# Optimization experiments

Measured on AMD Instinct MI355X. Metric: run time of the kernel, lower is better.

The kernel has to match this reference:

```python
import jax, jax.numpy as jnp
import numpy as np

N_NODES = 40000
N_EDGES = 640000
IN_CH = 128
HID_CH = 128
BN_EPS = 1e-5


def setup_inputs() -> dict:
    key = jax.random.key(0)
    k_x, k_ei, k_w, k_g = jax.random.split(key, 4)
    x = jax.random.normal(k_x, (N_NODES, IN_CH), dtype=jnp.float32)
    edge_index = jax.random.randint(k_ei, (2, N_EDGES), 0, N_NODES, dtype=jnp.int32)
    # Glorot init for GCNConv weight, zero bias (PyG defaults)
    limit = float(np.sqrt(6.0 / (IN_CH + HID_CH)))
    W = jax.random.uniform(k_w, (IN_CH, HID_CH), dtype=jnp.float32, minval=-limit, maxval=limit)
    b = jnp.zeros((HID_CH,), dtype=jnp.float32)
    gamma = jnp.ones((HID_CH,), dtype=jnp.float32)
    beta = jnp.zeros((HID_CH,), dtype=jnp.float32)
    return {"x": x, "edge_index": edge_index, "W": W, "b": b, "gamma": gamma, "beta": beta}


def reference(x, edge_index, W, b, gamma, beta):
    N = x.shape[0]
    src, dst = edge_index[0], edge_index[1]

    # --- GCNConv: h = x @ W, symmetric-normalized aggregation with self-loops ---
    h = x @ W  # [N, H]
    ones = jnp.ones((src.shape[0],), dtype=x.dtype)
    deg = jax.ops.segment_sum(ones, dst, num_segments=N) + 1.0  # +1 for self-loop
    dinv = jax.lax.rsqrt(deg)  # deg >= 1 always
    norm = dinv[src] * dinv[dst]  # [E]
    msg = h[src] * norm[:, None]  # [E, H] gather
    agg = jax.ops.segment_sum(msg, dst, num_segments=N)  # scatter-add
    agg = agg + h * (dinv * dinv)[:, None]  # self-loop contribution
    out = agg + b  # bias added after aggregation (PyG GCNConv)

    # --- BatchNorm1d (training mode: batch stats, biased variance) ---
    mean = jnp.mean(out, axis=0)
    var = jnp.mean((out - mean) ** 2, axis=0)
    out = gamma * (out - mean) * jax.lax.rsqrt(var + BN_EPS) + beta

    # --- ReLU (dropout is a no-op in eval) ---
    return jax.nn.relu(out)
```

## Files before the change

kernel.cpp:

```cpp
#include <hip/hip_runtime.h>

#define N_NODES 40000
#define N_EDGES 640000
#define CH 128
#define BN_EPS 1e-5f
#define CAP 48
#define CNT_S 8
#define MM_ROWS 80
#define MM_BLOCKS (N_NODES / MM_ROWS)
#define FILL_BLOCKS (N_EDGES / 1024)


typedef __bf16 bf16x8 __attribute__((ext_vector_type(8)));
typedef float f32x4 __attribute__((ext_vector_type(4)));

__device__ __forceinline__ float bf_lo(unsigned u) { return __uint_as_float(u << 16); }
__device__ __forceinline__ float bf_hi(unsigned u) { return __uint_as_float(u & 0xffff0000u); }
__device__ __forceinline__ unsigned short f2bf(float f) {
    unsigned u = __float_as_uint(f);
    unsigned r = 0x7fffu + ((u >> 16) & 1u);
    return (unsigned short)((u + r) >> 16);
}
__device__ __forceinline__ unsigned pack2bf(float a, float b) {
    return (unsigned)f2bf(a) | ((unsigned)f2bf(b) << 16);
}

__global__ __launch_bounds__(256) void mm_fill_kernel(const float* __restrict__ x,
                                                      const float* __restrict__ W,
                                                      unsigned short* __restrict__ hbf,
                                                      const int* __restrict__ src,
                                                      const int* __restrict__ dst,
                                                      int* __restrict__ cnt,
                                                      unsigned short* __restrict__ bucket16) {
    __shared__ unsigned xl[MM_ROWS * 68];
    int t = threadIdx.x;
    int bb = blockIdx.x;
    if (bb < FILL_BLOCKS) {
        int base = cnt[N_NODES * CNT_S];
        int4 dd = ((const int4*)dst)[bb * 256 + t];
        int4 ss = ((const int4*)src)[bb * 256 + t];
        int d[4] = {dd.x, dd.y, dd.z, dd.w};
        int s[4] = {ss.x, ss.y, ss.z, ss.w};
        int slot[4];
#pragma unroll
        for (int k = 0; k < 4; ++k) slot[k] = atomicAdd(&cnt[d[k] * CNT_S], 1) - base;
#pragma unroll
        for (int k = 0; k < 4; ++k)
            if (slot[k] < CAP) bucket16[d[k] * CAP + slot[k]] = (unsigned short)s[k];
        return;
    }
    int mb = bb - FILL_BLOCKS;
    size_t row0 = (size_t)mb * MM_ROWS;
#pragma unroll
    for (int it = 0; it < MM_ROWS * 32 / 256; ++it) {
        int idx = it * 256 + t;
        int row = idx >> 5, c4 = idx & 31;
        float4 f = ((const float4*)(x + (row0 + row) * CH))[c4];
        uint2 p;
        p.x = pack2bf(f.x, f.y);
        p.y = pack2bf(f.z, f.w);
        *(uint2*)&xl[row * 68 + 2 * c4] = p;
    }
    int w = t >> 6, l = t & 63;
    int q = l >> 4, c15 = l & 15;
    int ct0 = 2 * w, ct1 = 2 * w + 1;
    bf16x8 bf0[4], bf1[4];
#pragma unroll
    for (int ks = 0; ks < 4; ++ks) {
        const float* wp = W + (size_t)(ks * 32 + 8 * q) * CH + c15;
        float v0[8], v1[8];
#pragma unroll
        for (int j = 0; j < 8; ++j) {
            v0[j] = wp[j * CH + ct0 * 16];
            v1[j] = wp[j * CH + ct1 * 16];
        }
        uint4 u0, u1;
        u0.x = pack2bf(v0[0], v0[1]); u0.y = pack2bf(v0[2], v0[3]);
        u0.z = pack2bf(v0[4], v0[5]); u0.w = pack2bf(v0[6], v0[7]);
        u1.x = pack2bf(v1[0], v1[1]); u1.y = pack2bf(v1[2], v1[3]);
        u1.z = pack2bf(v1[4], v1[5]); u1.w = pack2bf(v1[6], v1[7]);
        bf0[ks] = __builtin_bit_cast(bf16x8, u0);
        bf1[ks] = __builtin_bit_cast(bf16x8, u1);
    }
    __syncthreads();
    for (int rt = 0; rt < MM_ROWS / 16; ++rt) {
        int rbase = rt * 16 + c15;
        f32x4 acc0 = {0.f, 0.f, 0.f, 0.f};
        f32x4 acc1 = {0.f, 0.f, 0.f, 0.f};
#pragma unroll
        for (int ks = 0; ks < 4; ++ks) {
            uint4 ua = *(const uint4*)&xl[rbase * 68 + ks * 16 + 4 * q];
            bf16x8 af = __builtin_bit_cast(bf16x8, ua);
            acc0 = __builtin_amdgcn_mfma_f32_16x16x32_bf16(af, bf0[ks], acc0, 0, 0, 0);
            acc1 = __builtin_amdgcn_mfma_f32_16x16x32_bf16(af, bf1[ks], acc1, 0, 0, 0);
        }
        unsigned short* hr = hbf + (row0 + rt * 16 + q * 4) * CH;
#pragma unroll
        for (int r = 0; r < 4; ++r) {
            hr[r * CH + ct0 * 16 + c15] = f2bf(acc0[r]);
            hr[r * CH + ct1 * 16 + c15] = f2bf(acc1[r]);
        }
    }
}

__global__ __launch_bounds__(256) void aggregate_kernel(const unsigned short* __restrict__ bucket16,
                                                        const int* __restrict__ cnt,
                                                        const unsigned short* __restrict__ hbf,
                                                        const float* __restrict__ b,
                                                        float* __restrict__ out,
                                                        float* __restrict__ sums32) {
    __shared__ float bsum[CH], bsq[CH];
    int t = threadIdx.x;
    if (t < CH) { bsum[t] = 0.0f; bsq[t] = 0.0f; }
    __syncthreads();
    int base = cnt[N_NODES * CNT_S];
    int wid = t >> 6;
    int lane = t & 63;
    int quarter = lane >> 4;
    int ql = lane & 15;
    const uint4* h4 = (const uint4*)hbf;
    float4 bv0 = ((const float4*)b)[ql * 2];
    float4 bv1 = ((const float4*)b)[ql * 2 + 1];
    int n_base = blockIdx.x * 16 + wid * 4;
    float s0 = 0, s1 = 0, s2 = 0, s3 = 0, s4 = 0, s5 = 0, s6 = 0, s7 = 0;
    float q0 = 0, q1 = 0, q2 = 0, q3 = 0, q4 = 0, q5 = 0, q6 = 0, q7 = 0;
#pragma unroll 1
    for (int it = 0; it < 4; ++it) {
        int n = n_base + it;
        int cn = cnt[n * CNT_S] - base;
        int m = cn < CAP ? cn : CAP;
        float dn = rsqrtf((float)cn + 1.0f);
        unsigned sx_pre = (lane < m) ? (unsigned)bucket16[n * CAP + lane] : 0u;
        float a0 = 0, a1 = 0, a2 = 0, a3 = 0, a4 = 0, a5 = 0, a6 = 0, a7 = 0;
        for (int jj = 0; jj < m; jj += 16) {
            int e = jj + quarter * 4;
            unsigned sx0 = (unsigned)__shfl((int)sx_pre, e, 64);
            unsigned sx1 = (unsigned)__shfl((int)sx_pre, e + 1, 64);
            unsigned sx2 = (unsigned)__shfl((int)sx_pre, e + 2, 64);
            unsigned sx3 = (unsigned)__shfl((int)sx_pre, e + 3, 64);
            int c0g = cnt[sx0 * CNT_S];
            int c1g = cnt[sx1 * CNT_S];
            int c2g = cnt[sx2 * CNT_S];
            int c3g = cnt[sx3 * CNT_S];
            uint4 r0 = h4[(size_t)sx0 * 16 + ql];
            uint4 r1 = h4[(size_t)sx1 * 16 + ql];
            uint4 r2 = h4[(size_t)sx2 * 16 + ql];
            uint4 r3 = h4[(size_t)sx3 * 16 + ql];
            float d0 = (e     < m) ? rsqrtf((float)(c0g - base) + 1.0f) : 0.0f;
            float d1 = (e + 1 < m) ? rsqrtf((float)(c1g - base) + 1.0f) : 0.0f;
            float d2 = (e + 2 < m) ? rsqrtf((float)(c2g - base) + 1.0f) : 0.0f;
            float d3 = (e + 3 < m) ? rsqrtf((float)(c3g - base) + 1.0f) : 0.0f;
            a0 += bf_lo(r0.x) * d0; a1 += bf_hi(r0.x) * d0;
            a2 += bf_lo(r0.y) * d0; a3 += bf_hi(r0.y) * d0;
            a4 += bf_lo(r0.z) * d0; a5 += bf_hi(r0.z) * d0;
            a6 += bf_lo(r0.w) * d0; a7 += bf_hi(r0.w) * d0;
            a0 += bf_lo(r1.x) * d1; a1 += bf_hi(r1.x) * d1;
            a2 += bf_lo(r1.y) * d1; a3 += bf_hi(r1.y) * d1;
            a4 += bf_lo(r1.z) * d1; a5 += bf_hi(r1.z) * d1;
            a6 += bf_lo(r1.w) * d1; a7 += bf_hi(r1.w) * d1;
            a0 += bf_lo(r2.x) * d2; a1 += bf_hi(r2.x) * d2;
            a2 += bf_lo(r2.y) * d2; a3 += bf_hi(r2.y) * d2;
            a4 += bf_lo(r2.z) * d2; a5 += bf_hi(r2.z) * d2;
            a6 += bf_lo(r2.w) * d2; a7 += bf_hi(r2.w) * d2;
            a0 += bf_lo(r3.x) * d3; a1 += bf_hi(r3.x) * d3;
            a2 += bf_lo(r3.y) * d3; a3 += bf_hi(r3.y) * d3;
            a4 += bf_lo(r3.z) * d3; a5 += bf_hi(r3.z) * d3;
            a6 += bf_lo(r3.w) * d3; a7 += bf_hi(r3.w) * d3;
        }
        a0 += __shfl_xor(a0, 16, 64); a0 += __shfl_xor(a0, 32, 64);
        a1 += __shfl_xor(a1, 16, 64); a1 += __shfl_xor(a1, 32, 64);
        a2 += __shfl_xor(a2, 16, 64); a2 += __shfl_xor(a2, 32, 64);
        a3 += __shfl_xor(a3, 16, 64); a3 += __shfl_xor(a3, 32, 64);
        a4 += __shfl_xor(a4, 16, 64); a4 += __shfl_xor(a4, 32, 64);
        a5 += __shfl_xor(a5, 16, 64); a5 += __shfl_xor(a5, 32, 64);
        a6 += __shfl_xor(a6, 16, 64); a6 += __shfl_xor(a6, 32, 64);
        a7 += __shfl_xor(a7, 16, 64); a7 += __shfl_xor(a7, 32, 64);
        if (quarter == 0) {
            uint4 raw = h4[(size_t)n * 16 + ql];
            float sq = dn * dn;
            float o0 = a0 * dn + bf_lo(raw.x) * sq + bv0.x;
            float o1 = a1 * dn + bf_hi(raw.x) * sq + bv0.y;
            float o2 = a2 * dn + bf_lo(raw.y) * sq + bv0.z;
            float o3 = a3 * dn + bf_hi(raw.y) * sq + bv0.w;
            float o4 = a4 * dn + bf_lo(raw.z) * sq + bv1.x;
            float o5 = a5 * dn + bf_hi(raw.z) * sq + bv1.y;
            float o6 = a6 * dn + bf_lo(raw.w) * sq + bv1.z;
            float o7 = a7 * dn + bf_hi(raw.w) * sq + bv1.w;
            float4* op = (float4*)(out + (size_t)n * CH + ql * 8);
            float4 w0 = {o0, o1, o2, o3};
            float4 w1 = {o4, o5, o6, o7};
            op[0] = w0;
            op[1] = w1;
            s0 += o0; q0 += o0 * o0;
            s1 += o1; q1 += o1 * o1;
            s2 += o2; q2 += o2 * o2;
            s3 += o3; q3 += o3 * o3;
            s4 += o4; q4 += o4 * o4;
            s5 += o5; q5 += o5 * o5;
            s6 += o6; q6 += o6 * o6;
            s7 += o7; q7 += o7 * o7;
        }
    }
    if (quarter == 0) {
        int c0 = ql * 8;
        atomicAdd(&bsum[c0 + 0], s0); atomicAdd(&bsq[c0 + 0], q0);
        atomicAdd(&bsum[c0 + 1], s1); atomicAdd(&bsq[c0 + 1], q1);
        atomicAdd(&bsum[c0 + 2], s2); atomicAdd(&bsq[c0 + 2], q2);
        atomicAdd(&bsum[c0 + 3], s3); atomicAdd(&bsq[c0 + 3], q3);
        atomicAdd(&bsum[c0 + 4], s4); atomicAdd(&bsq[c0 + 4], q4);
        atomicAdd(&bsum[c0 + 5], s5); atomicAdd(&bsq[c0 + 5], q5);
        atomicAdd(&bsum[c0 + 6], s6); atomicAdd(&bsq[c0 + 6], q6);
        atomicAdd(&bsum[c0 + 7], s7); atomicAdd(&bsq[c0 + 7], q7);
    }
    __syncthreads();
    atomicAdd(&sums32[(blockIdx.x & 31) * 256 + t], (t < CH) ? bsum[t] : bsq[t - CH]);
}

__global__ __launch_bounds__(256) void bn_relu_kernel(float* __restrict__ out,
                                                      const float* __restrict__ sums32,
                                                      const float* __restrict__ gamma,
                                                      const float* __restrict__ beta) {
    __shared__ float sc[CH], sh[CH];
    int t = threadIdx.x;
    if (t < CH) {
        float P = sums32[32 * 256];
        float s = -32.0f * P, q = -32.0f * P;
#pragma unroll
        for (int k = 0; k < 32; ++k) {
            s += sums32[k * 256 + t];
            q += sums32[k * 256 + CH + t];
        }
        const float invN = 1.0f / (float)N_NODES;
        float mean = s * invN;
        float var = q * invN - mean * mean;
        float scale = gamma[t] * rsqrtf(var + BN_EPS);
        sc[t] = scale;
        sh[t] = beta[t] - mean * scale;
    }
    __syncthreads();
    int i = blockIdx.x * 256 + t;
    int c0 = (i & 31) * 4;
    float4 v = ((float4*)out)[i];
    float r0 = v.x * sc[c0] + sh[c0];
    float r1 = v.y * sc[c0 + 1] + sh[c0 + 1];
    float r2 = v.z * sc[c0 + 2] + sh[c0 + 2];
    float r3 = v.w * sc[c0 + 3] + sh[c0 + 3];
    v.x = r0 > 0.0f ? r0 : 0.0f;
    v.y = r1 > 0.0f ? r1 : 0.0f;
    v.z = r2 > 0.0f ? r2 : 0.0f;
    v.w = r3 > 0.0f ? r3 : 0.0f;
    ((float4*)out)[i] = v;
}

extern "C" void kernel_launch(void* const* d_in, const int* in_sizes, int n_in,
                              void* d_out, int out_size, void* d_ws, size_t ws_size,
                              hipStream_t stream) {
    const float* x = (const float*)d_in[0];
    const int* ei = (const int*)d_in[1];
    const float* W = (const float*)d_in[2];
    const float* b = (const float*)d_in[3];
    const float* gamma = (const float*)d_in[4];
    const float* beta = (const float*)d_in[5];
    float* out = (float*)d_out;
    const int* src = ei;
    const int* dst = ei + N_EDGES;
    char* ws = (char*)d_ws;

    unsigned short* hbf = (unsigned short*)ws;
    int* cnt = (int*)(ws + 10240000);
    float* sums32 = (float*)(ws + 11520256);
    unsigned short* bucket16 = (unsigned short*)(ws + 11553280);

    mm_fill_kernel<<<FILL_BLOCKS + MM_BLOCKS, 256, 0, stream>>>(x, W, hbf, src, dst, cnt,
                                                                bucket16);
    aggregate_kernel<<<N_NODES / 16, 256, 0, stream>>>(bucket16, cnt, hbf, b, out, sums32);
    bn_relu_kernel<<<N_NODES * CH / 4 / 256, 256, 0, stream>>>(out, sums32, gamma, beta);
}
```

Measured before the change: 162.3 us.

## Split fused matmul/fill kernel into separate launches with smaller tiles

Splits the combined matmul and edge-bucket fill kernel into two separate kernels launched back to back. The matmul tile shrinks from 80 to 32 rows per block, which gives more blocks, and its row loop is unrolled. The fill kernel now handles 2 edges per thread with scalar loads instead of 4 with int4 loads. This removes branch divergence between the two roles in one grid and gives more blocks for occupancy, but it adds a kernel launch and loses any overlap between the two phases.

Result: slower. 167.2 us (+3.1%).

```diff
diff --git a/kernel.cpp b/kernel.cpp
--- a/kernel.cpp
+++ b/kernel.cpp
@@ -6,9 +6,9 @@
 #define BN_EPS 1e-5f
 #define CAP 48
 #define CNT_S 8
-#define MM_ROWS 80
+#define MM_ROWS 32
 #define MM_BLOCKS (N_NODES / MM_ROWS)
-#define FILL_BLOCKS (N_EDGES / 1024)
+#define FILL_BLOCKS (N_EDGES / 512)
 
 
 typedef __bf16 bf16x8 __attribute__((ext_vector_type(8)));
@@ -25,32 +25,13 @@
     return (unsigned)f2bf(a) | ((unsigned)f2bf(b) << 16);
 }
 
-__global__ __launch_bounds__(256) void mm_fill_kernel(const float* __restrict__ x,
-                                                      const float* __restrict__ W,
-                                                      unsigned short* __restrict__ hbf,
-                                                      const int* __restrict__ src,
-                                                      const int* __restrict__ dst,
-                                                      int* __restrict__ cnt,
-                                                      unsigned short* __restrict__ bucket16) {
+__global__ __launch_bounds__(256) void mm_kernel(const float* __restrict__ x,
+                                                 const float* __restrict__ W,
+                                                 unsigned short* __restrict__ hbf) {
     __shared__ unsigned xl[MM_ROWS * 68];
     int t = threadIdx.x;
     int bb = blockIdx.x;
-    if (bb < FILL_BLOCKS) {
-        int base = cnt[N_NODES * CNT_S];
-        int4 dd = ((const int4*)dst)[bb * 256 + t];
-        int4 ss = ((const int4*)src)[bb * 256 + t];
-        int d[4] = {dd.x, dd.y, dd.z, dd.w};
-        int s[4] = {ss.x, ss.y, ss.z, ss.w};
-        int slot[4];
-#pragma unroll
-        for (int k = 0; k < 4; ++k) slot[k] = atomicAdd(&cnt[d[k] * CNT_S], 1) - base;
-#pragma unroll
-        for (int k = 0; k < 4; ++k)
-            if (slot[k] < CAP) bucket16[d[k] * CAP + slot[k]] = (unsigned short)s[k];
-        return;
-    }
-    int mb = bb - FILL_BLOCKS;
-    size_t row0 = (size_t)mb * MM_ROWS;
+    size_t row0 = (size_t)bb * MM_ROWS;
 #pragma unroll
     for (int it = 0; it < MM_ROWS * 32 / 256; ++it) {
         int idx = it * 256 + t;
@@ -83,6 +64,7 @@
         bf1[ks] = __builtin_bit_cast(bf16x8, u1);
     }
     __syncthreads();
+#pragma unroll
     for (int rt = 0; rt < MM_ROWS / 16; ++rt) {
         int rbase = rt * 16 + c15;
         f32x4 acc0 = {0.f, 0.f, 0.f, 0.f};
@@ -101,6 +83,23 @@
             hr[r * CH + ct1 * 16 + c15] = f2bf(acc1[r]);
         }
     }
+}
+
+__global__ __launch_bounds__(256) void fill_kernel(const int* __restrict__ src,
+                                                   const int* __restrict__ dst,
+                                                   int* __restrict__ cnt,
+                                                   unsigned short* __restrict__ bucket16) {
+    int t = threadIdx.x;
+    int bb = blockIdx.x;
+    int base = cnt[N_NODES * CNT_S];
+    int i0 = bb * 512 + t;
+    int i1 = i0 + 256;
+    int d0 = dst[i0], d1 = dst[i1];
+    int s0 = src[i0], s1 = src[i1];
+    int sl0 = atomicAdd(&cnt[d0 * CNT_S], 1) - base;
+    int sl1 = atomicAdd(&cnt[d1 * CNT_S], 1) - base;
+    if (sl0 < CAP) bucket16[d0 * CAP + sl0] = (unsigned short)s0;
+    if (sl1 < CAP) bucket16[d1 * CAP + sl1] = (unsigned short)s1;
 }
 
 __global__ __launch_bounds__(256) void aggregate_kernel(const unsigned short* __restrict__ bucket16,
@@ -271,8 +270,8 @@
     float* sums32 = (float*)(ws + 11520256);
     unsigned short* bucket16 = (unsigned short*)(ws + 11553280);
 
-    mm_fill_kernel<<<FILL_BLOCKS + MM_BLOCKS, 256, 0, stream>>>(x, W, hbf, src, dst, cnt,
-                                                                bucket16);
+    mm_kernel<<<MM_BLOCKS, 256, 0, stream>>>(x, W, hbf);
+    fill_kernel<<<FILL_BLOCKS, 256, 0, stream>>>(src, dst, cnt, bucket16);
     aggregate_kernel<<<N_NODES / 16, 256, 0, stream>>>(bucket16, cnt, hbf, b, out, sums32);
     bn_relu_kernel<<<N_NODES * CH / 4 / 256, 256, 0, stream>>>(out, sums32, gamma, beta);
 }
```
